# Kernel optimization log

Hardware: AMD Instinct MI355X
Metric: run time of the kernel (lower is better)

Reference implementation:

```python
import jax, jax.numpy as jnp
import numpy as np
import math

EMBED_DIM = 1024
NUM_HEADS = 16
HEAD_DIM = EMBED_DIM // NUM_HEADS


def setup_inputs() -> dict:
    key = jax.random.key(0)
    k_x, k_wqkv, k_bqkv, k_wo, k_bo = jax.random.split(key, 5)
    bound_qkv = 1.0 / math.sqrt(EMBED_DIM)
    x = jax.random.normal(k_x, (32, 512, EMBED_DIM), dtype=jnp.float32)
    W_qkv = jax.random.uniform(k_wqkv, (3 * EMBED_DIM, EMBED_DIM), minval=-bound_qkv, maxval=bound_qkv, dtype=jnp.float32)
    b_qkv = jax.random.uniform(k_bqkv, (3 * EMBED_DIM,), minval=-bound_qkv, maxval=bound_qkv, dtype=jnp.float32)
    W_out = jax.random.uniform(k_wo, (EMBED_DIM, EMBED_DIM), minval=-bound_qkv, maxval=bound_qkv, dtype=jnp.float32)
    b_out = jax.random.uniform(k_bo, (EMBED_DIM,), minval=-bound_qkv, maxval=bound_qkv, dtype=jnp.float32)
    return {"x": x, "W_qkv": W_qkv, "b_qkv": b_qkv, "W_out": W_out, "b_out": b_out}


def reference(x, W_qkv, b_qkv, W_out, b_out):
    B, T, C = x.shape
    H, Dh = NUM_HEADS, HEAD_DIM
    # qkv projection: [B, T, 3C]
    qkv = jnp.einsum('btc,oc->bto', x, W_qkv) + b_qkv
    # NOTE: original views as (B, T, H, 3*Dh) then chunks last dim -> per-head
    # interleaved q/k/v layout; replicate exactly.
    qkv = qkv.reshape(B, T, H, 3 * Dh)
    q, k, v = jnp.split(qkv, 3, axis=-1)  # each [B, T, H, Dh]
    scale = 1.0 / math.sqrt(Dh)
    # scores [B, H, T, T]
    att = jnp.einsum('bqhd,bkhd->bhqk', q, k) * scale
    causal = jnp.tril(jnp.ones((T, T), dtype=bool))
    att = jnp.where(causal[None, None], att, -jnp.inf)
    att = jax.nn.softmax(att, axis=-1)
    # dropout p=0.0 -> identity (eval mode)
    y = jnp.einsum('bhqk,bkhd->bqhd', att, v).reshape(B, T, C)
    return jnp.einsum('btc,oc->bto', y, W_out) + b_out
```

## Files before the change

kernel.cpp:

```cpp
#include <hip/hip_runtime.h>

typedef __attribute__((ext_vector_type(8))) _Float16 f16x8;
typedef __attribute__((ext_vector_type(4))) _Float16 f16x4;
typedef __attribute__((ext_vector_type(4))) float f32x4;

#define NB 32
#define NT 512
#define NC 1024
#define NH 16
#define ND 64
#define NM (NB*NT)
#define N3 (3*NC)

#define AS1 __attribute__((address_space(1)))
#define AS3 __attribute__((address_space(3)))

__device__ __forceinline__ void gload_lds16(const void* g, void* l) {
  __builtin_amdgcn_global_load_lds((const AS1 unsigned int*)g,
                                   (AS3 unsigned int*)l, 16, 0, 0);
}

__global__ __launch_bounds__(256)
void split16(const float* __restrict__ in, _Float16* __restrict__ hi,
             _Float16* __restrict__ lo, int n8)
{
  int i = blockIdx.x*256 + threadIdx.x;
  const int stride = gridDim.x*256;
  for (; i < n8; i += stride) {
    f32x4 a = ((const f32x4*)in)[2*i];
    f32x4 b = ((const f32x4*)in)[2*i+1];
    f16x8 h, l;
#pragma unroll
    for (int j = 0; j < 4; ++j) {
      _Float16 h1 = (_Float16)a[j];
      h[j] = h1; l[j] = (_Float16)(a[j] - (float)h1);
      _Float16 h2 = (_Float16)b[j];
      h[j+4] = h2; l[j+4] = (_Float16)(b[j] - (float)h2);
    }
    ((f16x8*)hi)[i] = h;
    ((f16x8*)lo)[i] = l;
  }
}

template<int EPI>
__global__ __launch_bounds__(256, 2)
void gemm_f16(const _Float16* __restrict__ Ah, const _Float16* __restrict__ Al,
              const _Float16* __restrict__ Bh, const _Float16* __restrict__ Bl,
              const float* __restrict__ bias,
              void* __restrict__ O0, void* __restrict__ O1,
              void* __restrict__ O2, int K, int N)
{
  __shared__ _Float16 sAh[128*32], sAl[128*32], sBh[128*32], sBl[128*32];
  const int tid = threadIdx.x, lane = tid & 63, w = tid >> 6;
  const int wr = w >> 1, wc = w & 1;
  const int l15 = lane & 15, g = lane >> 4;
  const int tb = blockIdx.x, ob = blockIdx.y;

  const f32x4 zero = {0.f, 0.f, 0.f, 0.f};
  f32x4 acc[4][4];
#pragma unroll
  for (int i = 0; i < 4; ++i)
#pragma unroll
    for (int j = 0; j < 4; ++j) acc[i][j] = zero;

  const int srow = lane >> 2;
  const int skc  = (lane & 3) * 8;

  for (int k0 = 0; k0 < K; k0 += 32) {
#pragma unroll
    for (int r = 0; r < 2; ++r) {
      const int seg = r*4 + w;
      const int row = seg*16 + srow;
      const size_t ga = (size_t)(tb*128 + row)*K + k0 + skc;
      const size_t gb = (size_t)(ob*128 + row)*K + k0 + skc;
      gload_lds16(Ah + ga, &sAh[seg*512]);
      gload_lds16(Al + ga, &sAl[seg*512]);
      gload_lds16(Bh + gb, &sBh[seg*512]);
      gload_lds16(Bl + gb, &sBl[seg*512]);
    }
    __syncthreads();

    f16x8 bh[4], bl[4];
#pragma unroll
    for (int nj = 0; nj < 4; ++nj) {
      const int rb = (wc*64 + nj*16 + l15)*64 + g*16;
      bh[nj] = *(const f16x8*)((const char*)sBh + rb);
      bl[nj] = *(const f16x8*)((const char*)sBl + rb);
    }
#pragma unroll
    for (int mi = 0; mi < 4; ++mi) {
      const int ra = (wr*64 + mi*16 + l15)*64 + g*16;
      f16x8 ah = *(const f16x8*)((const char*)sAh + ra);
      f16x8 al = *(const f16x8*)((const char*)sAl + ra);
#pragma unroll
      for (int nj = 0; nj < 4; ++nj) {
        acc[mi][nj] = __builtin_amdgcn_mfma_f32_16x16x32_f16(ah, bh[nj], acc[mi][nj], 0, 0, 0);
        acc[mi][nj] = __builtin_amdgcn_mfma_f32_16x16x32_f16(ah, bl[nj], acc[mi][nj], 0, 0, 0);
        acc[mi][nj] = __builtin_amdgcn_mfma_f32_16x16x32_f16(al, bh[nj], acc[mi][nj], 0, 0, 0);
      }
    }
    __syncthreads();
  }

#pragma unroll
  for (int mi = 0; mi < 4; ++mi) {
#pragma unroll
    for (int nj = 0; nj < 4; ++nj) {
#pragma unroll
      for (int r = 0; r < 4; ++r) {
        const int trow = tb*128 + wr*64 + mi*16 + g*4 + r;
        const int ocol = ob*128 + wc*64 + nj*16 + l15;
        const float val = acc[mi][nj][r] + bias[ocol];
        if (EPI == 0) {
          const int h  = ocol / 192;
          const int rr = ocol - h*192;
          const int b  = trow >> 9, tt = trow & 511;
          const size_t base = (((size_t)(b*NH + h))*NT + tt)*ND;
          const _Float16 hv = (_Float16)val;
          if (rr < 64)       ((_Float16*)O0)[base + rr] = hv;
          else if (rr < 128) ((_Float16*)O1)[base + rr - 64] = hv;
          else               ((_Float16*)O2)[base + rr - 128] = hv;
        } else {
          ((float*)O0)[(size_t)trow * N + ocol] = val;
        }
      }
    }
  }
}

__global__ __launch_bounds__(256, 2)
void attn_f16(const _Float16* __restrict__ Qg, const _Float16* __restrict__ Kg,
              const _Float16* __restrict__ Vg,
              _Float16* __restrict__ Yh, _Float16* __restrict__ Yl)
{
  __shared__ _Float16 sK[64*64];
  __shared__ _Float16 sV[64*64];
  __shared__ _Float16 sP[128*64];

  const int tid = threadIdx.x, lane = tid & 63, w = tid >> 6;
  const int l15 = lane & 15, g = lane >> 4;
  const int bh = blockIdx.x, qt = blockIdx.y, qb = qt*128;
  const size_t hb = (size_t)bh * NT * ND;

  f16x8 qf[2][2];
  {
    const _Float16* qp = Qg + hb + (size_t)(qb + w*32 + l15)*ND;
#pragma unroll
    for (int nj = 0; nj < 2; ++nj)
#pragma unroll
      for (int ks = 0; ks < 2; ++ks)
        qf[nj][ks] = *(const f16x8*)(qp + nj*16*ND + ks*32 + g*8);
  }

  const f32x4 zero = {0.f, 0.f, 0.f, 0.f};
  f32x4 yacc[2][4];
#pragma unroll
  for (int m = 0; m < 2; ++m)
#pragma unroll
    for (int n = 0; n < 4; ++n) yacc[m][n] = zero;
  float lrun[2] = {0.f, 0.f};

  const int vrq = tid & 15;
  const int vc0 = (tid >> 4) * 4;

  const int nkt = 2*qt + 2;
  for (int kt = 0; kt < nkt; ++kt) {
    const int kb = kt*64;
    __syncthreads();
#pragma unroll
    for (int r = 0; r < 2; ++r) {
      const int seg = r*4 + w;
      const int row = seg*8 + (lane >> 3);
      const int gs  = (lane & 7) ^ (row & 7);
      gload_lds16(Kg + hb + (size_t)(kb + row)*ND + gs*8, &sK[seg*512]);
    }
    {
      const _Float16* vp = Vg + hb + (size_t)(kb + vrq*4)*ND + vc0;
      f16x4 v0 = *(const f16x4*)(vp);
      f16x4 v1 = *(const f16x4*)(vp + ND);
      f16x4 v2 = *(const f16x4*)(vp + 2*ND);
      f16x4 v3 = *(const f16x4*)(vp + 3*ND);
#pragma unroll
      for (int j = 0; j < 4; ++j) {
        const int d = vc0 + j;
        f16x4 t = { v0[j], v1[j], v2[j], v3[j] };
        const int byte = d*128 + ((((vrq>>1) ^ (d&7))) << 4) + ((vrq&1) << 3);
        *(f16x4*)((char*)sV + byte) = t;
      }
    }
    __syncthreads();

    f32x4 st[4][2];
#pragma unroll
    for (int mi = 0; mi < 4; ++mi)
#pragma unroll
      for (int nj = 0; nj < 2; ++nj) st[mi][nj] = zero;
#pragma unroll
    for (int ks = 0; ks < 2; ++ks)
#pragma unroll
      for (int mi = 0; mi < 4; ++mi) {
        const int kr = mi*16 + l15;
        const int byte = kr*128 + (((ks*4 + g) ^ (kr&7)) << 4);
        f16x8 kf = *(const f16x8*)((const char*)sK + byte);
#pragma unroll
        for (int nj = 0; nj < 2; ++nj)
          st[mi][nj] = __builtin_amdgcn_mfma_f32_16x16x32_f16(kf, qf[nj][ks], st[mi][nj], 0, 0, 0);
      }

    float lp[2] = {0.f, 0.f};
#pragma unroll
    for (int mi = 0; mi < 4; ++mi)
#pragma unroll
      for (int nj = 0; nj < 2; ++nj) {
        f16x4 ph;
#pragma unroll
        for (int r = 0; r < 4; ++r) {
          const int kk = kb + mi*16 + g*4 + r;
          const int qq = qb + w*32 + nj*16 + l15;
          const float p = (kk <= qq) ? __expf(st[mi][nj][r]*0.125f) : 0.0f;
          lp[nj] += p;
          ph[r] = (_Float16)p;
        }
        const int prow = w*32 + nj*16 + l15;
        const int slot = mi*2 + (g>>1);
        const int byte = prow*128 + (((slot ^ (prow&7))) << 4) + ((g&1) << 3);
        *(f16x4*)((char*)sP + byte) = ph;
      }
#pragma unroll
    for (int nj = 0; nj < 2; ++nj) {
      lp[nj] += __shfl_xor(lp[nj], 16);
      lp[nj] += __shfl_xor(lp[nj], 32);
      lrun[nj] += lp[nj];
    }

#pragma unroll
    for (int ks = 0; ks < 2; ++ks) {
      f16x8 pa[2];
#pragma unroll
      for (int m = 0; m < 2; ++m) {
        const int prow = w*32 + m*16 + l15;
        const int byte = prow*128 + (((ks*4 + g) ^ (prow&7)) << 4);
        pa[m] = *(const f16x8*)((const char*)sP + byte);
      }
#pragma unroll
      for (int n = 0; n < 4; ++n) {
        const int d = n*16 + l15;
        const int byte = d*128 + (((ks*4 + g) ^ (d&7)) << 4);
        f16x8 vf = *(const f16x8*)((const char*)sV + byte);
#pragma unroll
        for (int m = 0; m < 2; ++m)
          yacc[m][n] = __builtin_amdgcn_mfma_f32_16x16x32_f16(pa[m], vf, yacc[m][n], 0, 0, 0);
      }
    }
  }

  const int b = bh >> 4, h = bh & 15;
#pragma unroll
  for (int m = 0; m < 2; ++m)
#pragma unroll
    for (int r = 0; r < 4; ++r) {
      const float lv  = __shfl(lrun[m], g*4 + r);
      const float inv = 1.0f / lv;
      const int qrow  = qb + w*32 + m*16 + g*4 + r;
      const size_t base = ((size_t)(b*NT + qrow))*NC + h*ND;
#pragma unroll
      for (int n = 0; n < 4; ++n) {
        const float v = yacc[m][n][r] * inv;
        const _Float16 hv = (_Float16)v;
        Yh[base + n*16 + l15] = hv;
        Yl[base + n*16 + l15] = (_Float16)(v - (float)hv);
      }
    }
}

extern "C" void kernel_launch(void* const* d_in, const int* in_sizes, int n_in,
                              void* d_out, int out_size, void* d_ws, size_t ws_size,
                              hipStream_t stream)
{
  const float* x    = (const float*)d_in[0];
  const float* Wqkv = (const float*)d_in[1];
  const float* bqkv = (const float*)d_in[2];
  const float* Wout = (const float*)d_in[3];
  const float* bout = (const float*)d_in[4];
  float* out = (float*)d_out;

  char* p = (char*)d_ws;
  _Float16* xh  = (_Float16*)p; p += (size_t)NM*NC*2;
  _Float16* xl  = (_Float16*)p; p += (size_t)NM*NC*2;
  _Float16* wqh = (_Float16*)p; p += (size_t)N3*NC*2;
  _Float16* wql = (_Float16*)p; p += (size_t)N3*NC*2;
  _Float16* woh = (_Float16*)p; p += (size_t)NC*NC*2;
  _Float16* wol = (_Float16*)p; p += (size_t)NC*NC*2;
  _Float16* Qh  = (_Float16*)p; p += (size_t)NM*NC*2;
  _Float16* Kh  = (_Float16*)p; p += (size_t)NM*NC*2;
  _Float16* Vh  = (_Float16*)p; p += (size_t)NM*NC*2;
  _Float16* Yh  = (_Float16*)p; p += (size_t)NM*NC*2;
  _Float16* Yl  = (_Float16*)p; p += (size_t)NM*NC*2;

  split16<<<2048, 256, 0, stream>>>(x,    xh, xl, NM*NC/8);
  split16<<<1536, 256, 0, stream>>>(Wqkv, wqh, wql, N3*NC/8);
  split16<<<512,  256, 0, stream>>>(Wout, woh, wol, NC*NC/8);

  gemm_f16<0><<<dim3(NM/128, N3/128), 256, 0, stream>>>(
      xh, xl, wqh, wql, bqkv, Qh, Kh, Vh, NC, N3);
  attn_f16<<<dim3(NB*NH, 4), 256, 0, stream>>>(Qh, Kh, Vh, Yh, Yl);
  gemm_f16<1><<<dim3(NM/128, NC/128), 256, 0, stream>>>(
      Yh, Yl, woh, wol, bout, out, nullptr, nullptr, NC, NC);
}
```

Baseline: 594.0 us.

## Double-buffer GEMM LDS tiles and swizzle LDS layout to avoid bank conflicts

Doubles the shared-memory staging buffers so the next K-slice's global-to-LDS loads are issued before the current slice's MFMAs run, overlapping memory and compute. It also XOR-swizzles the 16-byte chunk column on both the load and read side so that fragment reads from LDS hit fewer bank conflicts. LDS usage doubles to 64KB per block, which may limit the two-blocks-per-CU occupancy target.

```diff
diff --git a/kernel.cpp b/kernel.cpp
--- a/kernel.cpp
+++ b/kernel.cpp
@@ -50,7 +50,7 @@
               void* __restrict__ O0, void* __restrict__ O1,
               void* __restrict__ O2, int K, int N)
 {
-  __shared__ _Float16 sAh[128*32], sAl[128*32], sBh[128*32], sBl[128*32];
+  __shared__ _Float16 smem[2][4][128*32];
   const int tid = threadIdx.x, lane = tid & 63, w = tid >> 6;
   const int wr = w >> 1, wc = w & 1;
   const int l15 = lane & 15, g = lane >> 4;
@@ -64,34 +64,49 @@
     for (int j = 0; j < 4; ++j) acc[i][j] = zero;
 
   const int srow = lane >> 2;
-  const int skc  = (lane & 3) * 8;
-
+  const int skc  = ((lane & 3) ^ ((lane >> 3) & 3))*8;
+  const int swz  = (g ^ ((l15 >> 1) & 3)) << 4;
+
+#define STAGE(buf, k0)                                                  \
+  {                                                                     \
+    _Pragma("unroll")                                                   \
+    for (int r = 0; r < 2; ++r) {                                       \
+      const int seg = r*4 + w;                                          \
+      const int row = seg*16 + srow;                                    \
+      const size_t ga = (size_t)(tb*128 + row)*K + (k0) + skc;          \
+      const size_t gb = (size_t)(ob*128 + row)*K + (k0) + skc;          \
+      gload_lds16(Ah + ga, &smem[buf][0][seg*512]);                     \
+      gload_lds16(Al + ga, &smem[buf][1][seg*512]);                     \
+      gload_lds16(Bh + gb, &smem[buf][2][seg*512]);                     \
+      gload_lds16(Bl + gb, &smem[buf][3][seg*512]);                     \
+    }                                                                   \
+  }
+
+  STAGE(0, 0)
+  asm volatile("s_waitcnt vmcnt(0)" ::: "memory");
+  __builtin_amdgcn_s_barrier();
+
+  int cur = 0;
   for (int k0 = 0; k0 < K; k0 += 32) {
-#pragma unroll
-    for (int r = 0; r < 2; ++r) {
-      const int seg = r*4 + w;
-      const int row = seg*16 + srow;
-      const size_t ga = (size_t)(tb*128 + row)*K + k0 + skc;
-      const size_t gb = (size_t)(ob*128 + row)*K + k0 + skc;
-      gload_lds16(Ah + ga, &sAh[seg*512]);
-      gload_lds16(Al + ga, &sAl[seg*512]);
-      gload_lds16(Bh + gb, &sBh[seg*512]);
-      gload_lds16(Bl + gb, &sBl[seg*512]);
-    }
-    __syncthreads();
+    if (k0 + 32 < K) STAGE(cur ^ 1, k0 + 32)
+
+    const char* cAh = (const char*)&smem[cur][0][0];
+    const char* cAl = (const char*)&smem[cur][1][0];
+    const char* cBh = (const char*)&smem[cur][2][0];
+    const char* cBl = (const char*)&smem[cur][3][0];
 
     f16x8 bh[4], bl[4];
 #pragma unroll
     for (int nj = 0; nj < 4; ++nj) {
-      const int rb = (wc*64 + nj*16 + l15)*64 + g*16;
-      bh[nj] = *(const f16x8*)((const char*)sBh + rb);
-      bl[nj] = *(const f16x8*)((const char*)sBl + rb);
+      const int rb = (wc*64 + nj*16 + l15)*64 + swz;
+      bh[nj] = *(const f16x8*)(cBh + rb);
+      bl[nj] = *(const f16x8*)(cBl + rb);
     }
 #pragma unroll
     for (int mi = 0; mi < 4; ++mi) {
-      const int ra = (wr*64 + mi*16 + l15)*64 + g*16;
-      f16x8 ah = *(const f16x8*)((const char*)sAh + ra);
-      f16x8 al = *(const f16x8*)((const char*)sAl + ra);
+      const int ra = (wr*64 + mi*16 + l15)*64 + swz;
+      f16x8 ah = *(const f16x8*)(cAh + ra);
+      f16x8 al = *(const f16x8*)(cAl + ra);
 #pragma unroll
       for (int nj = 0; nj < 4; ++nj) {
         acc[mi][nj] = __builtin_amdgcn_mfma_f32_16x16x32_f16(ah, bh[nj], acc[mi][nj], 0, 0, 0);
@@ -99,8 +114,11 @@
         acc[mi][nj] = __builtin_amdgcn_mfma_f32_16x16x32_f16(al, bh[nj], acc[mi][nj], 0, 0, 0);
       }
     }
-    __syncthreads();
-  }
+    asm volatile("s_waitcnt vmcnt(0) lgkmcnt(0)" ::: "memory");
+    __builtin_amdgcn_s_barrier();
+    cur ^= 1;
+  }
+#undef STAGE
 
 #pragma unroll
   for (int mi = 0; mi < 4; ++mi) {
```

New measurement: 570.5 us. 4.0% less time.
